# Kernel tuning notes

Hardware: AMD Instinct MI355X
Metric: run time of the kernel (lower is better)

## Reference

```python
import jax, jax.numpy as jnp
import numpy as np

B, L, M, D, H, FF, W = 2, 2048, 2048, 1024, 16, 4096, 64
DH = D // H


def _layernorm(x, g, b, eps=1e-5):
    mu = x.mean(-1, keepdims=True)
    var = ((x - mu) ** 2).mean(-1, keepdims=True)
    return (x - mu) / jnp.sqrt(var + eps) * g + b


def _mha(qx, kx, wq, bq, wk, bk, wv, bv, wo, bo, mask, bias):
    Bq, Lq, _ = qx.shape
    Lk = kx.shape[1]
    q = (qx @ wq + bq).reshape(Bq, Lq, H, DH).transpose(0, 2, 1, 3)  # [B,H,Lq,DH]
    k = (kx @ wk + bk).reshape(Bq, Lk, H, DH).transpose(0, 2, 1, 3)
    v = (kx @ wv + bv).reshape(Bq, Lk, H, DH).transpose(0, 2, 1, 3)
    s = jnp.einsum('bhqd,bhkd->bhqk', q, k) / jnp.sqrt(jnp.asarray(DH, qx.dtype))
    if bias is not None:
        s = s + bias[None]  # bias: [H,Lq,Lk]
    if mask is not None:
        s = jnp.where(mask[None, None], s, jnp.asarray(-1e9, qx.dtype))
    a = jax.nn.softmax(s, axis=-1)
    o = jnp.einsum('bhqk,bhkd->bhqd', a, v).transpose(0, 2, 1, 3).reshape(Bq, Lq, D)
    return o @ wo + bo


def _forward(x, mem,
             swq, sbq, swk, sbk, swv, sbv, swo, sbo,
             cwq, cbq, cwk, cbk, cwv, cbv, cwo, cbo,
             w1, b1, w2, b2,
             g1, be1, g2, be2, g3, be3):
    i = jnp.arange(L)[:, None]
    j = jnp.arange(L)[None, :]
    # causal local window mask: attend to j<=i with i-j < W
    mask = (j <= i) & ((i - j) < W)
    # ALiBi slopes for power-of-2 head counts: 2^{-8h/H}, h=1..H
    slopes = (2.0 ** (-8.0 * jnp.arange(1, H + 1, dtype=x.dtype) / H))
    bias = slopes[:, None, None] * (j - i).astype(x.dtype)[None]  # [H,L,L], <=0 on causal part
    sa = _mha(x, x, swq, sbq, swk, sbk, swv, sbv, swo, sbo, mask, bias)
    x = _layernorm(x + sa, g1, be1)
    # cross-attn mask is all ones -> no masking, no bias
    ca = _mha(x, mem, cwq, cbq, cwk, cbk, cwv, cbv, cwo, cbo, None, None)
    x = _layernorm(x + ca, g2, be2)
    ff = jax.nn.gelu(x @ w1 + b1, approximate=False) @ w2 + b2
    return _layernorm(x + ff, g3, be3)


def setup_inputs() -> dict:
    key = jax.random.key(0)
    ks = jax.random.split(key, 16)
    s = 0.02
    inp = {
        'x': jax.random.normal(ks[0], (B, L, D), jnp.float32),
        'mem': jax.random.normal(ks[1], (B, M, D), jnp.float32),
    }
    # self-attn params
    for n, k in zip(['swq', 'swk', 'swv', 'swo'], jax.random.split(ks[2], 4)):
        inp[n] = jax.random.normal(k, (D, D), jnp.float32) * s
    for n in ['sbq', 'sbk', 'sbv', 'sbo']:
        inp[n] = jnp.zeros((D,), jnp.float32)
    # cross-attn params
    for n, k in zip(['cwq', 'cwk', 'cwv', 'cwo'], jax.random.split(ks[3], 4)):
        inp[n] = jax.random.normal(k, (D, D), jnp.float32) * s
    for n in ['cbq', 'cbk', 'cbv', 'cbo']:
        inp[n] = jnp.zeros((D,), jnp.float32)
    # FFN params
    inp['w1'] = jax.random.normal(ks[4], (D, FF), jnp.float32) * s
    inp['b1'] = jnp.zeros((FF,), jnp.float32)
    inp['w2'] = jax.random.normal(ks[5], (FF, D), jnp.float32) * s
    inp['b2'] = jnp.zeros((D,), jnp.float32)
    # LayerNorm params
    for n in ['g1', 'g2', 'g3']:
        inp[n] = jnp.ones((D,), jnp.float32)
    for n in ['be1', 'be2', 'be3']:
        inp[n] = jnp.zeros((D,), jnp.float32)
    return inp


def reference(x, mem,
              swq, sbq, swk, sbk, swv, sbv, swo, sbo,
              cwq, cbq, cwk, cbk, cwv, cbv, cwo, cbo,
              w1, b1, w2, b2,
              g1, be1, g2, be2, g3, be3):
    return _forward(x, mem,
                    swq, sbq, swk, sbk, swv, sbv, swo, sbo,
                    cwq, cbq, cwk, cbk, cwv, cbv, cwo, cbo,
                    w1, b1, w2, b2,
                    g1, be1, g2, be2, g3, be3)
```

## Files before the change

kernel.cpp:

```cpp
#include <hip/hip_runtime.h>
#include <hip/hip_bf16.h>
#include <math.h>

#define Bc 2
#define Lc 2048
#define Mc 2048
#define Dc 1024
#define Hc 16
#define FFc 4096
#define DHc 64

typedef __bf16 bf16;
typedef float f32x4 __attribute__((ext_vector_type(4)));
typedef __bf16 bf16x8 __attribute__((ext_vector_type(8)));
typedef __bf16 bf16x4 __attribute__((ext_vector_type(4)));
typedef __bf16 bf16x2 __attribute__((ext_vector_type(2)));

__device__ inline void gload16(const bf16* g, const bf16* lds_base) {
  __builtin_amdgcn_global_load_lds(
      (const __attribute__((address_space(1))) void*)g,
      (__attribute__((address_space(3))) void*)lds_base, 16, 0, 0);
}

#define WAIT_VM(n) asm volatile("s_waitcnt vmcnt(" #n ")" ::: "memory")
#define WAIT_LGKM0 asm volatile("s_waitcnt lgkmcnt(0)" ::: "memory")
#define RAW_BAR() __builtin_amdgcn_s_barrier()
#define SCHED_FENCE() __builtin_amdgcn_sched_barrier(0)

__device__ inline float gelu_f(float v) {
  float u = 0.7978845608f * (v + 0.044715f * v * v * v);
  float e = exp2f(u * 2.885390082f);
  float th = 1.0f - 2.0f / (e + 1.0f);
  return 0.5f * v * (1.0f + th);
}

__global__ __launch_bounds__(256) void k_f2b(const float* __restrict__ in,
                                             bf16* __restrict__ out, long n4) {
  long i = (long)blockIdx.x * 256 + threadIdx.x;
  if (i >= n4) return;
  f32x4 v = *(const f32x4*)(in + i * 4);
  bf16x4 o;
  o[0] = (bf16)v[0]; o[1] = (bf16)v[1]; o[2] = (bf16)v[2]; o[3] = (bf16)v[3];
  *(bf16x4*)(out + i * 4) = o;
}

__global__ __launch_bounds__(256) void k_transpose_w(const float* __restrict__ in,
                                                     bf16* __restrict__ out,
                                                     int K, int N) {
  __shared__ float tile[64][65];
  int n0 = blockIdx.x * 64, k0 = blockIdx.y * 64;
  int t = threadIdx.x;
  int tr = t >> 4, tc = (t & 15) * 4;
#pragma unroll
  for (int p = 0; p < 4; p++) {
    int r = p * 16 + tr;
    f32x4 v = *(const f32x4*)(in + (long)(k0 + r) * N + n0 + tc);
    tile[r][tc] = v[0]; tile[r][tc + 1] = v[1];
    tile[r][tc + 2] = v[2]; tile[r][tc + 3] = v[3];
  }
  __syncthreads();
#pragma unroll
  for (int p = 0; p < 4; p++) {
    int rn = p * 16 + tr;
    bf16x4 o;
    o[0] = (bf16)tile[tc + 0][rn]; o[1] = (bf16)tile[tc + 1][rn];
    o[2] = (bf16)tile[tc + 2][rn]; o[3] = (bf16)tile[tc + 3][rn];
    *(bf16x4*)(out + (long)(n0 + rn) * K + k0 + tc) = o;
  }
}

__global__ __launch_bounds__(256) void k_transpose_v(const bf16* __restrict__ vb,
                                                     bf16* __restrict__ vt, int N) {
  __shared__ bf16 tile[64][72];
  int j0 = blockIdx.x * 64;
  int bh = blockIdx.y; int b = bh >> 4; int h = bh & 15;
  int t = threadIdx.x;
#pragma unroll
  for (int c = 0; c < 2; c++) {
    int id = t + c * 256;
    int r = id >> 3, c8 = (id & 7) * 8;
    *(bf16x8*)&tile[r][c8] =
        *(const bf16x8*)(vb + ((long)(b * N + j0 + r)) * Dc + h * DHc + c8);
  }
  __syncthreads();
#pragma unroll
  for (int c = 0; c < 2; c++) {
    int id = t + c * 256;
    int d = id >> 3, j8 = (id & 7) * 8;
    bf16x8 o;
#pragma unroll
    for (int e = 0; e < 8; e++) o[e] = tile[j8 + e][d];
    *(bf16x8*)(vt + ((long)bh * DHc + d) * N + j0 + j8) = o;
  }
}

__global__ __launch_bounds__(256) void k_gemm128(
    const bf16* __restrict__ A0, const bf16* __restrict__ A1,
    const bf16* __restrict__ A2, long lda,
    const bf16* __restrict__ B0, long bstride,
    bf16* __restrict__ outB, long ldc, long cstride,
    const float* __restrict__ bias0, const float* __restrict__ bias1,
    const float* __restrict__ bias2, int Kdim, int act, float scale0) {
  __shared__ __align__(16) bf16 As[2][128 * 64];
  __shared__ __align__(16) bf16 Bs[2][128 * 64];
  int z = blockIdx.z;
  const bf16* A = (z == 0) ? A0 : ((z == 1) ? A1 : A2);
  const bf16* Bt = B0 + (long)z * bstride;
  const float* bias = (z == 0) ? bias0 : ((z == 1) ? bias1 : bias2);
  float scl = (z == 0) ? scale0 : 1.0f;
  long cbase = (long)z * cstride;
  int bm = blockIdx.y * 128, bn = blockIdx.x * 128;
  int t = threadIdx.x, w = t >> 6, lane = t & 63;
  int wm = w >> 1, wn = w & 1;
  int lr = lane & 15, lg = lane >> 4;
  int srow = lane >> 3;
  int scol = (((lane & 7) * 16) ^ ((lane >> 3) << 4)) >> 1;
  f32x4 acc[4][4] = {};
  int nk = Kdim >> 6;
  auto stage = [&](int buf, int kt2) {
    long k0 = (long)kt2 * 64;
#pragma unroll
    for (int i = 0; i < 4; i++) {
      int row = (i * 4 + w) * 8 + srow;
      gload16(A + (long)(bm + row) * lda + k0 + scol, &As[buf][(i * 4 + w) * 512]);
      gload16(Bt + (long)(bn + row) * Kdim + k0 + scol, &Bs[buf][(i * 4 + w) * 512]);
    }
  };
  stage(0, 0);
  if (nk > 1) stage(1, 1);
  for (int kt = 0; kt < nk; ++kt) {
    int cur = kt & 1;
    if (kt + 1 < nk) { WAIT_VM(8); } else { WAIT_VM(0); }
    RAW_BAR();
    SCHED_FENCE();
    const char* pa = (const char*)&As[cur][0];
    const char* pb = (const char*)&Bs[cur][0];
    int xr = (lr & 7) << 4;
    bf16x8 af[2][4], bfr[2][4];
#pragma unroll
    for (int kk = 0; kk < 2; kk++) {
#pragma unroll
      for (int m = 0; m < 4; m++) {
        int row = wm * 64 + m * 16 + lr;
        af[kk][m] = *(const bf16x8*)(pa + (row << 7) + ((kk * 64 + lg * 16) ^ xr));
      }
#pragma unroll
      for (int n = 0; n < 4; n++) {
        int row = wn * 64 + n * 16 + lr;
        bfr[kk][n] = *(const bf16x8*)(pb + (row << 7) + ((kk * 64 + lg * 16) ^ xr));
      }
    }
    WAIT_LGKM0;
    SCHED_FENCE();
    RAW_BAR();
    if (kt + 2 < nk) stage(cur, kt + 2);
#pragma unroll
    for (int kk = 0; kk < 2; kk++)
#pragma unroll
      for (int m = 0; m < 4; m++)
#pragma unroll
        for (int n = 0; n < 4; n++)
          acc[m][n] = __builtin_amdgcn_mfma_f32_16x16x32_bf16(af[kk][m], bfr[kk][n],
                                                              acc[m][n], 0, 0, 0);
  }
#pragma unroll
  for (int n = 0; n < 4; n++) {
    int cg = bn + wn * 64 + n * 16 + lr;
    float bv = bias ? bias[cg] : 0.0f;
#pragma unroll
    for (int m = 0; m < 4; m++) {
#pragma unroll
      for (int rr = 0; rr < 4; rr++) {
        int rg = bm + wm * 64 + m * 16 + lg * 4 + rr;
        float v = (acc[m][n][rr] + bv) * scl;
        if (act == 1) v = gelu_f(v);
        outB[cbase + (long)rg * ldc + cg] = (bf16)v;
      }
    }
  }
}

__global__ __launch_bounds__(256) void k_gemmsk(
    const bf16* __restrict__ A, long lda,
    const bf16* __restrict__ Bt, int Kfull,
    float* __restrict__ psum, long slab, int Kchunk, int ldc) {
  __shared__ __align__(16) bf16 As[2][128 * 64];
  __shared__ __align__(16) bf16 Bs[2][128 * 64];
  int z = blockIdx.z;
  int bm = blockIdx.y * 128, bn = blockIdx.x * 128;
  int t = threadIdx.x, w = t >> 6, lane = t & 63;
  int wm = w >> 1, wn = w & 1;
  int lr = lane & 15, lg = lane >> 4;
  int srow = lane >> 3;
  int scol = (((lane & 7) * 16) ^ ((lane >> 3) << 4)) >> 1;
  f32x4 acc[4][4] = {};
  int nk = Kchunk >> 6;
  long kstart = (long)z * Kchunk;
  auto stage = [&](int buf, int kt2) {
    long k0 = kstart + (long)kt2 * 64;
#pragma unroll
    for (int i = 0; i < 4; i++) {
      int row = (i * 4 + w) * 8 + srow;
      gload16(A + (long)(bm + row) * lda + k0 + scol, &As[buf][(i * 4 + w) * 512]);
      gload16(Bt + (long)(bn + row) * Kfull + k0 + scol, &Bs[buf][(i * 4 + w) * 512]);
    }
  };
  stage(0, 0);
  if (nk > 1) stage(1, 1);
  for (int kt = 0; kt < nk; ++kt) {
    int cur = kt & 1;
    if (kt + 1 < nk) { WAIT_VM(8); } else { WAIT_VM(0); }
    RAW_BAR();
    SCHED_FENCE();
    const char* pa = (const char*)&As[cur][0];
    const char* pb = (const char*)&Bs[cur][0];
    int xr = (lr & 7) << 4;
    bf16x8 af[2][4], bfr[2][4];
#pragma unroll
    for (int kk = 0; kk < 2; kk++) {
#pragma unroll
      for (int m = 0; m < 4; m++) {
        int row = wm * 64 + m * 16 + lr;
        af[kk][m] = *(const bf16x8*)(pa + (row << 7) + ((kk * 64 + lg * 16) ^ xr));
      }
#pragma unroll
      for (int n = 0; n < 4; n++) {
        int row = wn * 64 + n * 16 + lr;
        bfr[kk][n] = *(const bf16x8*)(pb + (row << 7) + ((kk * 64 + lg * 16) ^ xr));
      }
    }
    WAIT_LGKM0;
    SCHED_FENCE();
    RAW_BAR();
    if (kt + 2 < nk) stage(cur, kt + 2);
#pragma unroll
    for (int kk = 0; kk < 2; kk++)
#pragma unroll
      for (int m = 0; m < 4; m++)
#pragma unroll
        for (int n = 0; n < 4; n++)
          acc[m][n] = __builtin_amdgcn_mfma_f32_16x16x32_bf16(af[kk][m], bfr[kk][n],
                                                              acc[m][n], 0, 0, 0);
  }
  float* po = psum + (long)z * slab;
#pragma unroll
  for (int n = 0; n < 4; n++) {
    int cg = bn + wn * 64 + n * 16 + lr;
#pragma unroll
    for (int m = 0; m < 4; m++) {
#pragma unroll
      for (int rr = 0; rr < 4; rr++) {
        int rg = bm + wm * 64 + m * 16 + lg * 4 + rr;
        po[(long)rg * ldc + cg] = acc[m][n][rr];
      }
    }
  }
}

template <int WINDOWED>
__global__ __launch_bounds__(256) void k_flash(const bf16* __restrict__ Qg,
                                               const bf16* __restrict__ Kg,
                                               const bf16* __restrict__ Vtg,
                                               bf16* __restrict__ Og, int nkv) {
  __shared__ __align__(16) bf16 Qs[64 * 64];
  __shared__ __align__(16) bf16 Ks[2][64 * 64];
  __shared__ __align__(16) bf16 Vs[2][64 * 64];
  int flat = blockIdx.y * 32 + blockIdx.x;
  int flat2 = (flat & 7) * 128 + (flat >> 3);
  int i0 = (flat2 & 31) * 64;
  int bh = flat2 >> 5;
  int b = bh >> 4, h = bh & 15;
  int t = threadIdx.x, w = t >> 6, lane = t & 63;
  int lr = lane & 15, lg = lane >> 4;
  long qoff = ((long)b * Lc + i0) * Dc + h * DHc;
  long koff = ((long)b * nkv) * Dc + h * DHc;
  long vtoff = (long)bh * DHc * nkv;
  int o0 = w * 1024 + (lane << 4), o1 = o0 + 4096;
  int r0 = o0 >> 7, c0 = (o0 & 127) ^ ((r0 & 7) << 4);
  int r1 = o1 >> 7, c1 = (o1 & 127) ^ ((r1 & 7) << 4);
  int d0 = c0 >> 1, d1 = c1 >> 1;
  gload16(Qg + qoff + (long)r0 * Dc + d0, &Qs[w * 512]);
  gload16(Qg + qoff + (long)r1 * Dc + d1, &Qs[2048 + w * 512]);
  int kb0 = WINDOWED ? (i0 >= 64 ? i0 - 64 : 0) : 0;
  int nt = WINDOWED ? ((i0 - kb0) >> 6) + 1 : (nkv >> 6);
  auto stage = [&](int buf, int kbase) {
    gload16(Kg + koff + (long)(kbase + r0) * Dc + d0, &Ks[buf][w * 512]);
    gload16(Kg + koff + (long)(kbase + r1) * Dc + d1, &Ks[buf][2048 + w * 512]);
    gload16(Vtg + vtoff + (long)r0 * nkv + kbase + d0, &Vs[buf][w * 512]);
    gload16(Vtg + vtoff + (long)r1 * nkv + kbase + d1, &Vs[buf][2048 + w * 512]);
  };
  stage(0, kb0);
  WAIT_VM(4);
  RAW_BAR();
  SCHED_FENCE();
  bf16x8 bq[2];
#pragma unroll
  for (int ks = 0; ks < 2; ks++) {
    int rq = w * 16 + lr, cb = ks * 64 + lg * 16;
    bq[ks] = *(const bf16x8*)&Qs[((rq << 7) + (cb ^ ((rq & 7) << 4))) >> 1];
  }
  char* pbase = (char*)&Qs[w * 1024];
  float mrun = -1e30f, lrun = 0.f;
  f32x4 oa[4] = {};
  float slopeL2 = WINDOWED ? exp2f(-0.5f * (float)(h + 1)) * 1.44269504f : 0.0f;
  int qabs = i0 + w * 16 + lr;
  for (int tch = 0; tch < nt; tch++) {
    int cur = tch & 1;
    if (tch + 1 < nt) {
      stage(cur ^ 1, kb0 + (tch + 1) * 64);
      WAIT_VM(4);
    } else {
      WAIT_VM(0);
    }
    RAW_BAR();
    SCHED_FENCE();
    int kbase = kb0 + tch * 64;
    f32x4 st[4] = {};
    __builtin_amdgcn_s_setprio(1);
#pragma unroll
    for (int ks = 0; ks < 2; ks++) {
#pragma unroll
      for (int m = 0; m < 4; m++) {
        int rk = m * 16 + lr, cb = ks * 64 + lg * 16;
        bf16x8 ka = *(const bf16x8*)&Ks[cur][((rk << 7) + (cb ^ ((rk & 7) << 4))) >> 1];
        st[m] = __builtin_amdgcn_mfma_f32_16x16x32_bf16(ka, bq[ks], st[m], 0, 0, 0);
      }
    }
    __builtin_amdgcn_s_setprio(0);
    float sc[4][4];
    float pmax = -3.0e38f;
#pragma unroll
    for (int m = 0; m < 4; m++)
#pragma unroll
      for (int rr = 0; rr < 4; rr++) {
        int kab = kbase + m * 16 + lg * 4 + rr;
        float v = st[m][rr];
        if (WINDOWED) {
          v += slopeL2 * (float)(kab - qabs);
          bool valid = (kab <= qabs) && (qabs - kab < 64);
          v = valid ? v : -3.0e38f;
        }
        sc[m][rr] = v;
        pmax = fmaxf(pmax, v);
      }
    pmax = fmaxf(pmax, __shfl_xor(pmax, 16));
    pmax = fmaxf(pmax, __shfl_xor(pmax, 32));
    float mx = mrun;
    if (!__all(pmax - mrun <= 8.0f)) {
      mx = fmaxf(mrun, pmax);
      float corr = exp2f(mrun - mx);
      mrun = mx;
      lrun *= corr;
      float cq[4];
#pragma unroll
      for (int rr = 0; rr < 4; rr++) cq[rr] = __shfl(corr, lg * 4 + rr);
#pragma unroll
      for (int jd = 0; jd < 4; jd++) {
        oa[jd][0] *= cq[0]; oa[jd][1] *= cq[1];
        oa[jd][2] *= cq[2]; oa[jd][3] *= cq[3];
      }
    }
    float ps = 0.f;
#pragma unroll
    for (int m = 0; m < 4; m++) {
#pragma unroll
      for (int hh = 0; hh < 2; hh++) {
        float p0 = exp2f(sc[m][2 * hh] - mx);
        float p1 = exp2f(sc[m][2 * hh + 1] - mx);
        ps += p0 + p1;
        bf16x2 pw; pw[0] = (bf16)p0; pw[1] = (bf16)p1;
        int kcol = m * 16 + lg * 4 + 2 * hh;
        *(bf16x2*)(pbase + (lr << 7) + (((kcol << 1)) ^ ((lr & 7) << 4))) = pw;
      }
    }
    lrun += ps;
    __builtin_amdgcn_s_setprio(1);
#pragma unroll
    for (int ks = 0; ks < 2; ks++) {
      bf16x8 pa = *(const bf16x8*)(pbase + (lr << 7) +
                                   (((ks * 64 + lg * 16)) ^ ((lr & 7) << 4)));
#pragma unroll
      for (int jd = 0; jd < 4; jd++) {
        int rv = jd * 16 + lr, cb = ks * 64 + lg * 16;
        bf16x8 vf = *(const bf16x8*)&Vs[cur][((rv << 7) + (cb ^ ((rv & 7) << 4))) >> 1];
        oa[jd] = __builtin_amdgcn_mfma_f32_16x16x32_bf16(pa, vf, oa[jd], 0, 0, 0);
      }
    }
    __builtin_amdgcn_s_setprio(0);
    WAIT_LGKM0;
    SCHED_FENCE();
    RAW_BAR();
  }
  float ls = lrun + __shfl_xor(lrun, 16);
  ls += __shfl_xor(ls, 32);
  float inv = 1.0f / ls;
  float iq[4];
#pragma unroll
  for (int rr = 0; rr < 4; rr++) iq[rr] = __shfl(inv, lg * 4 + rr);
#pragma unroll
  for (int rr = 0; rr < 4; rr++) {
    int qo = i0 + w * 16 + lg * 4 + rr;
#pragma unroll
    for (int jd = 0; jd < 4; jd++)
      Og[((long)b * Lc + qo) * Dc + h * DHc + jd * 16 + lr] =
          (bf16)(oa[jd][rr] * iq[rr]);
  }
}

template <int NS>
__global__ __launch_bounds__(256) void k_lnred(const float* __restrict__ psum,
                                               long slab,
                                               const float* __restrict__ bias,
                                               const float* __restrict__ addsrc,
                                               const float* __restrict__ g,
                                               const float* __restrict__ bb,
                                               float* __restrict__ outF,
                                               bf16* __restrict__ outB) {
  long row = blockIdx.x;
  int t = threadIdx.x; int lane = t & 63; int wid = t >> 6;
  __shared__ float red[8];
  f32x4 v = *(const f32x4*)(psum + row * Dc + t * 4);
#pragma unroll
  for (int s = 1; s < NS; s++) {
    f32x4 u = *(const f32x4*)(psum + s * slab + row * Dc + t * 4);
    v[0] += u[0]; v[1] += u[1]; v[2] += u[2]; v[3] += u[3];
  }
  f32x4 bv = *(const f32x4*)(bias + t * 4);
  f32x4 av = *(const f32x4*)(addsrc + row * Dc + t * 4);
  v[0] += bv[0] + av[0]; v[1] += bv[1] + av[1];
  v[2] += bv[2] + av[2]; v[3] += bv[3] + av[3];
  float s = v[0] + v[1] + v[2] + v[3];
  float s2 = v[0] * v[0] + v[1] * v[1] + v[2] * v[2] + v[3] * v[3];
#pragma unroll
  for (int off = 1; off < 64; off <<= 1) {
    s += __shfl_xor(s, off);
    s2 += __shfl_xor(s2, off);
  }
  if (lane == 0) { red[wid] = s; red[4 + wid] = s2; }
  __syncthreads();
  s = red[0] + red[1] + red[2] + red[3];
  s2 = red[4] + red[5] + red[6] + red[7];
  float mu = s * (1.0f / Dc);
  float var = s2 * (1.0f / Dc) - mu * mu;
  float rs = rsqrtf(var + 1e-5f);
#pragma unroll
  for (int e = 0; e < 4; e++) {
    int c = t * 4 + e;
    float y = (v[e] - mu) * rs * g[c] + bb[c];
    if (outF) outF[row * Dc + c] = y;
    if (outB) outB[row * Dc + c] = (bf16)y;
  }
}

extern "C" void kernel_launch(void* const* d_in, const int* in_sizes, int n_in,
                              void* d_out, int out_size, void* d_ws,
                              size_t ws_size, hipStream_t stream) {
  (void)in_sizes; (void)n_in; (void)out_size; (void)ws_size;
  const float* x = (const float*)d_in[0];
  const float* mem = (const float*)d_in[1];
  const float* swq = (const float*)d_in[2];
  const float* swk = (const float*)d_in[3];
  const float* swv = (const float*)d_in[4];
  const float* swo = (const float*)d_in[5];
  const float* sbq = (const float*)d_in[6];
  const float* sbk = (const float*)d_in[7];
  const float* sbv = (const float*)d_in[8];
  const float* sbo = (const float*)d_in[9];
  const float* cwq = (const float*)d_in[10];
  const float* cwk = (const float*)d_in[11];
  const float* cwv = (const float*)d_in[12];
  const float* cwo = (const float*)d_in[13];
  const float* cbq = (const float*)d_in[14];
  const float* cbk = (const float*)d_in[15];
  const float* cbv = (const float*)d_in[16];
  const float* cbo = (const float*)d_in[17];
  const float* w1 = (const float*)d_in[18];
  const float* b1 = (const float*)d_in[19];
  const float* w2 = (const float*)d_in[20];
  const float* b2 = (const float*)d_in[21];
  const float* g1 = (const float*)d_in[22];
  const float* g2 = (const float*)d_in[23];
  const float* g3 = (const float*)d_in[24];
  const float* be1 = (const float*)d_in[25];
  const float* be2 = (const float*)d_in[26];
  const float* be3 = (const float*)d_in[27];
  float* out = (float*)d_out;

  char* ws = (char*)d_ws;
  size_t off = 0;
  auto alloc = [&](size_t bytes) -> char* {
    char* p = ws + off;
    off = (off + bytes + 255) & ~(size_t)255;
    return p;
  };

  const long BL = (long)Bc * Lc;
  const long BM = (long)Bc * Mc;
  const long DD = (long)Dc * Dc;
  const long SL = BL * Dc;
  const float QSCL = 0.125f * 1.44269504f;

  bf16* wT0 = (bf16*)alloc((size_t)8 * DD * 2);
  bf16* w1T = (bf16*)alloc((size_t)FFc * Dc * 2);
  bf16* w2T = (bf16*)alloc((size_t)Dc * FFc * 2);
  bf16* xb = (bf16*)alloc((size_t)BL * Dc * 2);
  bf16* memb = (bf16*)alloc((size_t)BM * Dc * 2);
  bf16* x1b = (bf16*)alloc((size_t)BL * Dc * 2);
  bf16* x2b = (bf16*)alloc((size_t)BL * Dc * 2);
  bf16* qb = (bf16*)alloc((size_t)BL * Dc * 2);
  bf16* kb = (bf16*)alloc((size_t)BM * Dc * 2);
  bf16* vb = (bf16*)alloc((size_t)BM * Dc * 2);
  bf16* ob = (bf16*)alloc((size_t)BL * Dc * 2);
  bf16* vtS = (bf16*)alloc((size_t)Bc * Hc * DHc * Lc * 2);
  bf16* vtC = (bf16*)alloc((size_t)Bc * Hc * DHc * Mc * 2);
  float* x1f = (float*)alloc((size_t)BL * Dc * 4);
  float* x2f = (float*)alloc((size_t)BL * Dc * 4);
  bf16* ffh = (bf16*)alloc((size_t)BL * FFc * 2);
  float* psum = (float*)alloc((size_t)4 * SL * 4);

  const float* wsrc[8] = {swq, swk, swv, swo, cwq, cwk, cwv, cwo};
  for (int i = 0; i < 8; i++)
    k_transpose_w<<<dim3(Dc / 64, Dc / 64), 256, 0, stream>>>(wsrc[i], wT0 + i * DD, Dc, Dc);
  k_transpose_w<<<dim3(FFc / 64, Dc / 64), 256, 0, stream>>>(w1, w1T, Dc, FFc);
  k_transpose_w<<<dim3(Dc / 64, FFc / 64), 256, 0, stream>>>(w2, w2T, FFc, Dc);
  k_f2b<<<dim3((unsigned)(BL * Dc / 4 / 256)), 256, 0, stream>>>(x, xb, BL * Dc / 4);
  k_f2b<<<dim3((unsigned)(BM * Dc / 4 / 256)), 256, 0, stream>>>(mem, memb, BM * Dc / 4);

  k_gemm128<<<dim3(Dc / 128, BL / 128, 3), 256, 0, stream>>>(
      xb, xb, xb, Dc, wT0, DD, qb, Dc, SL, sbq, sbk, sbv, Dc, 0, QSCL);
  k_transpose_v<<<dim3(Lc / 64, Bc * Hc), 256, 0, stream>>>(vb, vtS, Lc);
  k_flash<1><<<dim3(Lc / 64, Bc * Hc), 256, 0, stream>>>(qb, kb, vtS, ob, Lc);
  k_gemmsk<<<dim3(Dc / 128, BL / 128, 2), 256, 0, stream>>>(
      ob, Dc, wT0 + 3 * DD, Dc, psum, SL, 512, Dc);
  k_lnred<2><<<dim3((unsigned)BL), 256, 0, stream>>>(psum, SL, sbo, x, g1, be1,
                                                     x1f, x1b);

  k_gemm128<<<dim3(Dc / 128, BM / 128, 3), 256, 0, stream>>>(
      x1b, memb, memb, Dc, wT0 + 4 * DD, DD, qb, Dc, SL, cbq, cbk, cbv, Dc, 0, QSCL);
  k_transpose_v<<<dim3(Mc / 64, Bc * Hc), 256, 0, stream>>>(vb, vtC, Mc);
  k_flash<0><<<dim3(Lc / 64, Bc * Hc), 256, 0, stream>>>(qb, kb, vtC, ob, Mc);
  k_gemmsk<<<dim3(Dc / 128, BL / 128, 2), 256, 0, stream>>>(
      ob, Dc, wT0 + 7 * DD, Dc, psum, SL, 512, Dc);
  k_lnred<2><<<dim3((unsigned)BL), 256, 0, stream>>>(psum, SL, cbo, x1f, g2, be2,
                                                     x2f, x2b);

  k_gemm128<<<dim3(FFc / 128, BL / 128, 1), 256, 0, stream>>>(
      x2b, x2b, x2b, Dc, w1T, 0, ffh, FFc, 0, b1, b1, b1, Dc, 1, 1.0f);
  k_gemmsk<<<dim3(Dc / 128, BL / 128, 4), 256, 0, stream>>>(
      ffh, FFc, w2T, FFc, psum, SL, 1024, Dc);
  k_lnred<4><<<dim3((unsigned)BL), 256, 0, stream>>>(psum, SL, b2, x2f, g3, be3,
                                                     out, nullptr);
}
```

Before: 413.3 us.

## Split GEMM LDS reads to overlap with MFMA, remap blocks across XCDs, batch weight transposes

In both GEMM kernels the inner loop now issues LDS reads for the two k-halves separately. It waits only for the first half before starting MFMAs on it, then issues the next global prefetch and runs the second half, so LDS latency overlaps with matrix math. Workgroup indices are remapped so consecutive tiles land on the same XCD, aiming for better L2 reuse. The eight DxD weight transposes are merged into one launch to cut launch overhead, and the flash kernel gets small ILP tweaks (a max-reduction chain and split partial sums). The remap assumes the workgroup count divides by 8, and the wait counts depend on exact instruction ordering.

```diff
diff --git a/kernel.cpp b/kernel.cpp
--- a/kernel.cpp
+++ b/kernel.cpp
@@ -16,6 +16,8 @@
 typedef __bf16 bf16x4 __attribute__((ext_vector_type(4)));
 typedef __bf16 bf16x2 __attribute__((ext_vector_type(2)));
 
+struct Ptrs8 { const float* p[8]; };
+
 __device__ inline void gload16(const bf16* g, const bf16* lds_base) {
   __builtin_amdgcn_global_load_lds(
       (const __attribute__((address_space(1))) void*)g,
@@ -23,7 +25,7 @@
 }
 
 #define WAIT_VM(n) asm volatile("s_waitcnt vmcnt(" #n ")" ::: "memory")
-#define WAIT_LGKM0 asm volatile("s_waitcnt lgkmcnt(0)" ::: "memory")
+#define WAIT_LGKM(n) asm volatile("s_waitcnt lgkmcnt(" #n ")" ::: "memory")
 #define RAW_BAR() __builtin_amdgcn_s_barrier()
 #define SCHED_FENCE() __builtin_amdgcn_sched_barrier(0)
 
@@ -32,6 +34,11 @@
   float e = exp2f(u * 2.885390082f);
   float th = 1.0f - 2.0f / (e + 1.0f);
   return 0.5f * v * (1.0f + th);
+}
+
+__device__ inline int xcd_remap(int flat, int nwg) {
+  int cpx = nwg >> 3;
+  return (flat & 7) * cpx + (flat >> 3);
 }
 
 __global__ __launch_bounds__(256) void k_f2b(const float* __restrict__ in,
@@ -42,6 +49,32 @@
   bf16x4 o;
   o[0] = (bf16)v[0]; o[1] = (bf16)v[1]; o[2] = (bf16)v[2]; o[3] = (bf16)v[3];
   *(bf16x4*)(out + i * 4) = o;
+}
+
+__global__ __launch_bounds__(256) void k_transpose_w8(Ptrs8 srcs,
+                                                      bf16* __restrict__ out) {
+  __shared__ float tile[64][65];
+  const float* in = srcs.p[blockIdx.z];
+  bf16* o = out + (long)blockIdx.z * Dc * Dc;
+  int n0 = blockIdx.x * 64, k0 = blockIdx.y * 64;
+  int t = threadIdx.x;
+  int tr = t >> 4, tc = (t & 15) * 4;
+#pragma unroll
+  for (int p = 0; p < 4; p++) {
+    int r = p * 16 + tr;
+    f32x4 v = *(const f32x4*)(in + (long)(k0 + r) * Dc + n0 + tc);
+    tile[r][tc] = v[0]; tile[r][tc + 1] = v[1];
+    tile[r][tc + 2] = v[2]; tile[r][tc + 3] = v[3];
+  }
+  __syncthreads();
+#pragma unroll
+  for (int p = 0; p < 4; p++) {
+    int rn = p * 16 + tr;
+    bf16x4 ov;
+    ov[0] = (bf16)tile[tc + 0][rn]; ov[1] = (bf16)tile[tc + 1][rn];
+    ov[2] = (bf16)tile[tc + 2][rn]; ov[3] = (bf16)tile[tc + 3][rn];
+    *(bf16x4*)(o + (long)(n0 + rn) * Dc + k0 + tc) = ov;
+  }
 }
 
 __global__ __launch_bounds__(256) void k_transpose_w(const float* __restrict__ in,
@@ -103,13 +136,18 @@
     const float* __restrict__ bias2, int Kdim, int act, float scale0) {
   __shared__ __align__(16) bf16 As[2][128 * 64];
   __shared__ __align__(16) bf16 Bs[2][128 * 64];
-  int z = blockIdx.z;
+  int gx = gridDim.x, gy = gridDim.y;
+  int nwg = gx * gy * gridDim.z;
+  int flat = (blockIdx.z * gy + blockIdx.y) * gx + blockIdx.x;
+  int f2 = xcd_remap(flat, nwg);
+  int bxi = f2 % gx; int tmp = f2 / gx;
+  int byi = tmp % gy; int z = tmp / gy;
   const bf16* A = (z == 0) ? A0 : ((z == 1) ? A1 : A2);
   const bf16* Bt = B0 + (long)z * bstride;
   const float* bias = (z == 0) ? bias0 : ((z == 1) ? bias1 : bias2);
   float scl = (z == 0) ? scale0 : 1.0f;
   long cbase = (long)z * cstride;
-  int bm = blockIdx.y * 128, bn = blockIdx.x * 128;
+  int bm = byi * 128, bn = bxi * 128;
   int t = threadIdx.x, w = t >> 6, lane = t & 63;
   int wm = w >> 1, wn = w & 1;
   int lr = lane & 15, lg = lane >> 4;
@@ -138,30 +176,46 @@
     int xr = (lr & 7) << 4;
     bf16x8 af[2][4], bfr[2][4];
 #pragma unroll
-    for (int kk = 0; kk < 2; kk++) {
-#pragma unroll
-      for (int m = 0; m < 4; m++) {
-        int row = wm * 64 + m * 16 + lr;
-        af[kk][m] = *(const bf16x8*)(pa + (row << 7) + ((kk * 64 + lg * 16) ^ xr));
-      }
-#pragma unroll
-      for (int n = 0; n < 4; n++) {
-        int row = wn * 64 + n * 16 + lr;
-        bfr[kk][n] = *(const bf16x8*)(pb + (row << 7) + ((kk * 64 + lg * 16) ^ xr));
-      }
-    }
-    WAIT_LGKM0;
+    for (int m = 0; m < 4; m++) {
+      int row = wm * 64 + m * 16 + lr;
+      af[0][m] = *(const bf16x8*)(pa + (row << 7) + ((lg * 16) ^ xr));
+    }
+#pragma unroll
+    for (int n = 0; n < 4; n++) {
+      int row = wn * 64 + n * 16 + lr;
+      bfr[0][n] = *(const bf16x8*)(pb + (row << 7) + ((lg * 16) ^ xr));
+    }
+    SCHED_FENCE();
+#pragma unroll
+    for (int m = 0; m < 4; m++) {
+      int row = wm * 64 + m * 16 + lr;
+      af[1][m] = *(const bf16x8*)(pa + (row << 7) + ((64 + lg * 16) ^ xr));
+    }
+#pragma unroll
+    for (int n = 0; n < 4; n++) {
+      int row = wn * 64 + n * 16 + lr;
+      bfr[1][n] = *(const bf16x8*)(pb + (row << 7) + ((64 + lg * 16) ^ xr));
+    }
+    SCHED_FENCE();
+    WAIT_LGKM(8);
+    SCHED_FENCE();
+#pragma unroll
+    for (int m = 0; m < 4; m++)
+#pragma unroll
+      for (int n = 0; n < 4; n++)
+        acc[m][n] = __builtin_amdgcn_mfma_f32_16x16x32_bf16(af[0][m], bfr[0][n],
+                                                            acc[m][n], 0, 0, 0);
+    WAIT_LGKM(0);
     SCHED_FENCE();
     RAW_BAR();
     if (kt + 2 < nk) stage(cur, kt + 2);
-#pragma unroll
-    for (int kk = 0; kk < 2; kk++)
-#pragma unroll
-      for (int m = 0; m < 4; m++)
-#pragma unroll
-        for (int n = 0; n < 4; n++)
-          acc[m][n] = __builtin_amdgcn_mfma_f32_16x16x32_bf16(af[kk][m], bfr[kk][n],
-                                                              acc[m][n], 0, 0, 0);
+    SCHED_FENCE();
+#pragma unroll
+    for (int m = 0; m < 4; m++)
+#pragma unroll
+      for (int n = 0; n < 4; n++)
+        acc[m][n] = __builtin_amdgcn_mfma_f32_16x16x32_bf16(af[1][m], bfr[1][n],
+                                                            acc[m][n], 0, 0, 0);
   }
 #pragma unroll
   for (int n = 0; n < 4; n++) {
@@ -186,8 +240,13 @@
     float* __restrict__ psum, long slab, int Kchunk, int ldc) {
   __shared__ __align__(16) bf16 As[2][128 * 64];
   __shared__ __align__(16) bf16 Bs[2][128 * 64];
-  int z = blockIdx.z;
-  int bm = blockIdx.y * 128, bn = blockIdx.x * 128;
+  int gx = gridDim.x, gy = gridDim.y;
+  int nwg = gx * gy * gridDim.z;
+  int flat = (blockIdx.z * gy + blockIdx.y) * gx + blockIdx.x;
+  int f2 = xcd_remap(flat, nwg);
+  int bxi = f2 % gx; int tmp = f2 / gx;
+  int byi = tmp % gy; int z = tmp / gy;
+  int bm = byi * 128, bn = bxi * 128;
   int t = threadIdx.x, w = t >> 6, lane = t & 63;
   int wm = w >> 1, wn = w & 1;
   int lr = lane & 15, lg = lane >> 4;
@@ -217,30 +276,46 @@
     int xr = (lr & 7) << 4;
     bf16x8 af[2][4], bfr[2][4];
 #pragma unroll
-    for (int kk = 0; kk < 2; kk++) {
-#pragma unroll
-      for (int m = 0; m < 4; m++) {
-        int row = wm * 64 + m * 16 + lr;
-        af[kk][m] = *(const bf16x8*)(pa + (row << 7) + ((kk * 64 + lg * 16) ^ xr));
-      }
-#pragma unroll
-      for (int n = 0; n < 4; n++) {
-        int row = wn * 64 + n * 16 + lr;
-        bfr[kk][n] = *(const bf16x8*)(pb + (row << 7) + ((kk * 64 + lg * 16) ^ xr));
-      }
-    }
-    WAIT_LGKM0;
+    for (int m = 0; m < 4; m++) {
+      int row = wm * 64 + m * 16 + lr;
+      af[0][m] = *(const bf16x8*)(pa + (row << 7) + ((lg * 16) ^ xr));
+    }
+#pragma unroll
+    for (int n = 0; n < 4; n++) {
+      int row = wn * 64 + n * 16 + lr;
+      bfr[0][n] = *(const bf16x8*)(pb + (row << 7) + ((lg * 16) ^ xr));
+    }
+    SCHED_FENCE();
+#pragma unroll
+    for (int m = 0; m < 4; m++) {
+      int row = wm * 64 + m * 16 + lr;
+      af[1][m] = *(const bf16x8*)(pa + (row << 7) + ((64 + lg * 16) ^ xr));
+    }
+#pragma unroll
+    for (int n = 0; n < 4; n++) {
+      int row = wn * 64 + n * 16 + lr;
+      bfr[1][n] = *(const bf16x8*)(pb + (row << 7) + ((64 + lg * 16) ^ xr));
+    }
+    SCHED_FENCE();
+    WAIT_LGKM(8);
+    SCHED_FENCE();
+#pragma unroll
+    for (int m = 0; m < 4; m++)
+#pragma unroll
+      for (int n = 0; n < 4; n++)
+        acc[m][n] = __builtin_amdgcn_mfma_f32_16x16x32_bf16(af[0][m], bfr[0][n],
+                                                            acc[m][n], 0, 0, 0);
+    WAIT_LGKM(0);
     SCHED_FENCE();
     RAW_BAR();
     if (kt + 2 < nk) stage(cur, kt + 2);
-#pragma unroll
-    for (int kk = 0; kk < 2; kk++)
-#pragma unroll
-      for (int m = 0; m < 4; m++)
-#pragma unroll
-        for (int n = 0; n < 4; n++)
-          acc[m][n] = __builtin_amdgcn_mfma_f32_16x16x32_bf16(af[kk][m], bfr[kk][n],
-                                                              acc[m][n], 0, 0, 0);
+    SCHED_FENCE();
+#pragma unroll
+    for (int m = 0; m < 4; m++)
+#pragma unroll
+      for (int n = 0; n < 4; n++)
+        acc[m][n] = __builtin_amdgcn_mfma_f32_16x16x32_bf16(af[1][m], bfr[1][n],
+                                                            acc[m][n], 0, 0, 0);
   }
   float* po = psum + (long)z * slab;
 #pragma unroll
@@ -328,21 +403,27 @@
     }
     __builtin_amdgcn_s_setprio(0);
     float sc[4][4];
-    float pmax = -3.0e38f;
 #pragma unroll
     for (int m = 0; m < 4; m++)
 #pragma unroll
       for (int rr = 0; rr < 4; rr++) {
-        int kab = kbase + m * 16 + lg * 4 + rr;
         float v = st[m][rr];
         if (WINDOWED) {
+          int kab = kbase + m * 16 + lg * 4 + rr;
           v += slopeL2 * (float)(kab - qabs);
           bool valid = (kab <= qabs) && (qabs - kab < 64);
           v = valid ? v : -3.0e38f;
         }
         sc[m][rr] = v;
-        pmax = fmaxf(pmax, v);
       }
+    float pmax = fmaxf(fmaxf(sc[0][0], sc[0][1]), sc[0][2]);
+    pmax = fmaxf(fmaxf(pmax, sc[0][3]), sc[1][0]);
+    pmax = fmaxf(fmaxf(pmax, sc[1][1]), sc[1][2]);
+    pmax = fmaxf(fmaxf(pmax, sc[1][3]), sc[2][0]);
+    pmax = fmaxf(fmaxf(pmax, sc[2][1]), sc[2][2]);
+    pmax = fmaxf(fmaxf(pmax, sc[2][3]), sc[3][0]);
+    pmax = fmaxf(fmaxf(pmax, sc[3][1]), sc[3][2]);
+    pmax = fmaxf(pmax, sc[3][3]);
     pmax = fmaxf(pmax, __shfl_xor(pmax, 16));
     pmax = fmaxf(pmax, __shfl_xor(pmax, 32));
     float mx = mrun;
@@ -360,20 +441,20 @@
         oa[jd][2] *= cq[2]; oa[jd][3] *= cq[3];
       }
     }
-    float ps = 0.f;
+    float ps0 = 0.f, ps1 = 0.f;
 #pragma unroll
     for (int m = 0; m < 4; m++) {
 #pragma unroll
       for (int hh = 0; hh < 2; hh++) {
         float p0 = exp2f(sc[m][2 * hh] - mx);
         float p1 = exp2f(sc[m][2 * hh + 1] - mx);
-        ps += p0 + p1;
+        ps0 += p0; ps1 += p1;
         bf16x2 pw; pw[0] = (bf16)p0; pw[1] = (bf16)p1;
         int kcol = m * 16 + lg * 4 + 2 * hh;
         *(bf16x2*)(pbase + (lr << 7) + (((kcol << 1)) ^ ((lr & 7) << 4))) = pw;
       }
     }
-    lrun += ps;
+    lrun += ps0 + ps1;
     __builtin_amdgcn_s_setprio(1);
 #pragma unroll
     for (int ks = 0; ks < 2; ks++) {
@@ -387,7 +468,7 @@
       }
     }
     __builtin_amdgcn_s_setprio(0);
-    WAIT_LGKM0;
+    WAIT_LGKM(0);
     SCHED_FENCE();
     RAW_BAR();
   }
@@ -518,9 +599,10 @@
   bf16* ffh = (bf16*)alloc((size_t)BL * FFc * 2);
   float* psum = (float*)alloc((size_t)4 * SL * 4);
 
-  const float* wsrc[8] = {swq, swk, swv, swo, cwq, cwk, cwv, cwo};
-  for (int i = 0; i < 8; i++)
-    k_transpose_w<<<dim3(Dc / 64, Dc / 64), 256, 0, stream>>>(wsrc[i], wT0 + i * DD, Dc, Dc);
+  Ptrs8 srcs;
+  srcs.p[0] = swq; srcs.p[1] = swk; srcs.p[2] = swv; srcs.p[3] = swo;
+  srcs.p[4] = cwq; srcs.p[5] = cwk; srcs.p[6] = cwv; srcs.p[7] = cwo;
+  k_transpose_w8<<<dim3(Dc / 64, Dc / 64, 8), 256, 0, stream>>>(srcs, wT0);
   k_transpose_w<<<dim3(FFc / 64, Dc / 64), 256, 0, stream>>>(w1, w1T, Dc, FFc);
   k_transpose_w<<<dim3(Dc / 64, FFc / 64), 256, 0, stream>>>(w2, w2T, FFc, Dc);
   k_f2b<<<dim3((unsigned)(BL * Dc / 4 / 256)), 256, 0, stream>>>(x, xb, BL * Dc / 4);
```

New measurement: 383.4 us. 7.2% less time.
